# Performance work log

Hardware: AMD Instinct MI355X
Metric: run time of the kernel (lower is better)

## Reference

```python
import jax, jax.numpy as jnp
import numpy as np
import math

DIM = 768
NUM_HEADS = 12
HEAD_DIM = DIM // NUM_HEADS


def setup_inputs() -> dict:
    key = jax.random.key(0)
    k_x, k_q, k_k, k_v = jax.random.split(key, 4)
    s = 1.0 / math.sqrt(DIM)
    return {
        "x": jax.random.normal(k_x, (2, 2048, DIM), dtype=jnp.float32),
        "Wq": jax.random.normal(k_q, (DIM, DIM), dtype=jnp.float32) * s,
        "Wk": jax.random.normal(k_k, (DIM, DIM), dtype=jnp.float32) * s,
        "Wv": jax.random.normal(k_v, (DIM, DIM), dtype=jnp.float32) * s,
    }


def reference(x, Wq, Wk, Wv):
    b, n, _ = x.shape
    # nn.Linear(dim, dim, bias=False): y = x @ W.T
    def split_heads(y):
        return y.reshape(b, n, NUM_HEADS, HEAD_DIM).transpose(0, 2, 1, 3)  # b h n d
    Q = split_heads(x @ Wq.T)
    K = split_heads(x @ Wk.T)
    V = split_heads(x @ Wv.T)
    scores = jnp.einsum('bhqd,bhkd->bhqk', Q, K)
    # FAITHFUL to source: softmax over the HEADS axis (dim=1), then scale by 1/sqrt(dim)
    attn = jax.nn.softmax(scores, axis=1) / math.sqrt(DIM)
    out = jnp.einsum('bhqk,bhkd->bhqd', attn, V)
    out = out.transpose(0, 2, 1, 3).reshape(b, n, DIM)  # b n (h d)
    return out  # to_out is Identity (project_out=False)
```

## Files before the change

kernel.cpp:

```cpp
#include <hip/hip_runtime.h>

#define DIM 768
#define NHEADS 12
#define HDIM 64
#define BATCH 2
#define SEQ 2048
#define ROWS (BATCH*SEQ)
#define KSPLIT 4

typedef __attribute__((ext_vector_type(8))) _Float16 f16x8;
typedef __attribute__((ext_vector_type(4))) _Float16 f16x4;
typedef __attribute__((ext_vector_type(2))) _Float16 f16x2;
typedef __attribute__((ext_vector_type(4))) float    f32x4;

__device__ __forceinline__ void dma16(const _Float16* g, _Float16* l) {
    __builtin_amdgcn_global_load_lds(
        (const __attribute__((address_space(1))) unsigned int*)g,
        (__attribute__((address_space(3))) unsigned int*)l, 16, 0, 0);
}

__device__ __forceinline__ void barrier_lgkm() {
    asm volatile("s_waitcnt lgkmcnt(0)\n\ts_barrier" ::: "memory");
}


__global__ __launch_bounds__(256) void cvt_all(
    const float* __restrict__ x,  const float* __restrict__ wq,
    const float* __restrict__ wk, const float* __restrict__ wv,
    _Float16* __restrict__ xf,  _Float16* __restrict__ wqf,
    _Float16* __restrict__ wkf, _Float16* __restrict__ wvf)
{
    const int lane = threadIdx.x & 63;
    const int wid  = (blockIdx.x * 256 + threadIdx.x) >> 6;
    const float* src; _Float16* dst; int t;
    float sc = 1.0f;
    if (wid < 6144)      { src = x;  dst = xf;  t = wid;        }
    else if (wid < 7296) { src = wq; dst = wqf; t = wid - 6144; sc = 1.4426950408889634f; }
    else if (wid < 8448) { src = wk; dst = wkf; t = wid - 7296; }
    else                 { src = wv; dst = wvf; t = wid - 8448; }
    const int c = lane & 15, quad = lane >> 4;
    const int mt = t / 24, kt = t % 24;
    const float* p = src + (size_t)(mt*16 + c) * 768 + kt*32 + quad*8;
    float4 v0 = *(const float4*)p;
    float4 v1 = *(const float4*)(p + 4);
    f16x8 o;
    o[0]=(_Float16)(v0.x*sc); o[1]=(_Float16)(v0.y*sc); o[2]=(_Float16)(v0.z*sc); o[3]=(_Float16)(v0.w*sc);
    o[4]=(_Float16)(v1.x*sc); o[5]=(_Float16)(v1.y*sc); o[6]=(_Float16)(v1.z*sc); o[7]=(_Float16)(v1.w*sc);
    *reinterpret_cast<f16x8*>(dst + ((size_t)t * 64 + lane) * 8) = o;
}

__global__ __launch_bounds__(512) void gemm3(
    const _Float16* __restrict__ xf, const _Float16* __restrict__ wqkf,
    const _Float16* __restrict__ wvf,
    _Float16* __restrict__ Qf, _Float16* __restrict__ Kf, _Float16* __restrict__ Vkt)
{
    __shared__ _Float16 Ab[2][16*512];
    __shared__ _Float16 Bb[2][8*512];
    const int tid = threadIdx.x, lane = tid & 63, w = tid >> 6;
    const int c = lane & 15, quad = lane >> 4;

    const _Float16 *Af, *Bf;
    int mt0, nt0, mode;
    if ((int)blockIdx.x < 192) {
        int mt = blockIdx.x / 12, nt = blockIdx.x % 12;
        Af = xf; Bf = wqkf; mt0 = mt*16; nt0 = nt*8; mode = 0;
    } else {
        int v = blockIdx.x - 192;
        int mt = v / 32, nt = v % 32;
        Af = wvf; Bf = xf; mt0 = mt*16; nt0 = nt*8; mode = 1;
    }

    auto stage = [&](int kt, int buf) {
#pragma unroll
        for (int u = 0; u < 3; ++u) {
            const int cc = w*3 + u;
            const _Float16* s = (cc < 16) ? Af + ((size_t)(mt0+cc)*24 + kt)*512
                                          : Bf + ((size_t)(nt0+cc-16)*24 + kt)*512;
            _Float16* d = (cc < 16) ? &Ab[buf][cc*512] : &Bb[buf][(cc-16)*512];
            dma16(s + lane*8, d);
        }
    };

    stage(0, 0);
    __syncthreads();

    f32x4 acc[4][4] = {};
    for (int kt = 0; kt < 24; ++kt) {
        const int cur = kt & 1;
        if (kt < 23) stage(kt+1, cur^1);
        f16x8 a[4], b[4];
#pragma unroll
        for (int i = 0; i < 4; ++i)
            a[i] = *(const f16x8*)(&Ab[cur][((w>>1)*4 + i)*512] + lane*8);
#pragma unroll
        for (int j = 0; j < 4; ++j)
            b[j] = *(const f16x8*)(&Bb[cur][((w&1)*4 + j)*512] + lane*8);
#pragma unroll
        for (int i = 0; i < 4; ++i)
#pragma unroll
            for (int j = 0; j < 4; ++j)
                acc[i][j] = __builtin_amdgcn_mfma_f32_16x16x32_f16(a[i], b[j], acc[i][j], 0,0,0);
        __syncthreads();
    }

    _Float16* L = &Ab[0][0] + w*1280;
#pragma unroll
    for (int i2 = 0; i2 < 2; ++i2)
#pragma unroll
        for (int j2 = 0; j2 < 2; ++j2) {
#pragma unroll
            for (int ii = 0; ii < 2; ++ii)
#pragma unroll
                for (int jj = 0; jj < 2; ++jj)
#pragma unroll
                    for (int r = 0; r < 4; ++r)
                        L[(ii*16 + quad*4 + r)*40 + jj*16 + c] =
                            (_Float16)acc[i2*2+ii][j2*2+jj][r];
#pragma unroll
            for (int ii = 0; ii < 2; ++ii) {
                const int mtg = mt0 + (w>>1)*4 + i2*2 + ii;
                if (mode == 0) {
                    f16x8 v = *(const f16x8*)(L + (ii*16 + c)*40 + quad*8);
                    const int nt32 = (nt0 + (w&1)*4)/2 + j2;
                    _Float16* dst = (nt32 < 24)
                        ? Qf + ((size_t)(mtg*24 + nt32)*64 + lane)*8
                        : Kf + ((size_t)(mtg*24 + nt32 - 24)*64 + lane)*8;
                    *(f16x8*)dst = v;
                } else {
#pragma unroll
                    for (int jj = 0; jj < 2; ++jj) {
                        f16x4 v4 = *(const f16x4*)(L + (ii*16 + c)*40 + jj*16 + quad*4);
                        const int kcu = nt0 + (w&1)*4 + j2*2 + jj;
                        *(f16x4*)(Vkt + ((size_t)kcu*48 + mtg)*256 + lane*4) = v4;
                    }
                }
            }
        }
}

__global__ __launch_bounds__(512) __attribute__((amdgpu_waves_per_eu(4)))
void attn_kernel(
    const _Float16* __restrict__ Qf, const _Float16* __restrict__ Kf,
    const _Float16* __restrict__ Vkt,
    float* __restrict__ out,
    _Float16* __restrict__ part)
{
    __shared__ __attribute__((aligned(16))) float    Ps[8][336];
    __shared__ __attribute__((aligned(16))) _Float16 Pl[2][12][16][20];
    const int tid = threadIdx.x, lane = tid & 63, w = tid >> 6;
    const int c = lane & 15, quad = lane >> 4;
    const int qi = w >> 2, g = w & 3;

    const int bid = blockIdx.x;
    const int rb = (bid & 7)*64 + (bid >> 3);
    const int qb = rb & 63;
    const int ks = (rb >> 6) & 3;
    const int b  = rb >> 8;
    const int qrow0 = b*SEQ + qb*32;
    const int qt16  = (qrow0 >> 4) + qi;
    const int kb16  = (b*SEQ + ks*(SEQ/KSPLIT)) >> 4;
    const int psoff = quad*84 + c*4;

    f16x8 qreg[6];
#pragma unroll
    for (int u = 0; u < 6; ++u)
        qreg[u] = *(const f16x8*)(Qf + ((size_t)(qt16*24 + g*6 + u)*64 + lane)*8);

    const _Float16* Kp0 = Kf + ((size_t)kb16*24 + g*6)*512 + (size_t)lane*8;
    const _Float16* Vb0 = Vkt + ((size_t)kb16*48 + g)*256 + (size_t)lane*4;

    f32x4 o_acc[12] = {};
    f16x4 vv[12];
    f32x4 e3[3];

    for (int t = 0; t < 32; ++t) {
        const _Float16* Kpt = Kp0 + (size_t)t*24*512;
        f16x8 k0 = *(const f16x8*)(Kpt        );
        f16x8 k1 = *(const f16x8*)(Kpt +   512);
        f16x8 k2 = *(const f16x8*)(Kpt + 2*512);
        f16x8 k3 = *(const f16x8*)(Kpt + 3*512);
        f16x8 k4 = *(const f16x8*)(Kpt + 4*512);
        f16x8 k5 = *(const f16x8*)(Kpt + 5*512);
        {
            f32x4 a0 = {}, a1 = {}, a2 = {};
            a0 = __builtin_amdgcn_mfma_f32_16x16x32_f16(k0, qreg[0], a0, 0,0,0);
            a0 = __builtin_amdgcn_mfma_f32_16x16x32_f16(k1, qreg[1], a0, 0,0,0);
            a1 = __builtin_amdgcn_mfma_f32_16x16x32_f16(k2, qreg[2], a1, 0,0,0);
            a1 = __builtin_amdgcn_mfma_f32_16x16x32_f16(k3, qreg[3], a1, 0,0,0);
            a2 = __builtin_amdgcn_mfma_f32_16x16x32_f16(k4, qreg[4], a2, 0,0,0);
            a2 = __builtin_amdgcn_mfma_f32_16x16x32_f16(k5, qreg[5], a2, 0,0,0);
#pragma unroll
            for (int r = 0; r < 4; ++r) e3[0][r] = __builtin_amdgcn_exp2f(a0[r]);
#pragma unroll
            for (int r = 0; r < 4; ++r) e3[1][r] = __builtin_amdgcn_exp2f(a1[r]);
#pragma unroll
            for (int r = 0; r < 4; ++r) e3[2][r] = __builtin_amdgcn_exp2f(a2[r]);
        }
        {
            f32x4 ps;
#pragma unroll
            for (int r = 0; r < 4; ++r) ps[r] = e3[0][r] + e3[1][r] + e3[2][r];
            *(f32x4*)&Ps[qi*4+g][psoff] = ps;
        }
        if (t > 0) {
#pragma unroll
            for (int h = 0; h < 12; ++h) {
                f16x4 pf = *(const f16x4*)&Pl[qi][h][c][quad*4];
                o_acc[h] = __builtin_amdgcn_mfma_f32_16x16x16f16(vv[h], pf, o_acc[h], 0,0,0);
            }
        }
        barrier_lgkm();
#pragma unroll
        for (int h = 0; h < 12; ++h)
            vv[h] = *(const f16x4*)(Vb0 + ((size_t)t*48 + h*4)*256);
        {
            f32x4 s0 = *(const f32x4*)&Ps[qi*4+0][psoff];
            f32x4 s1 = *(const f32x4*)&Ps[qi*4+1][psoff];
            f32x4 s2 = *(const f32x4*)&Ps[qi*4+2][psoff];
            f32x4 s3 = *(const f32x4*)&Ps[qi*4+3][psoff];
            f32x4 inv;
#pragma unroll
            for (int r = 0; r < 4; ++r)
                inv[r] = __builtin_amdgcn_rcpf(
                    (s0[r]+s1[r]+s2[r]+s3[r]) * 27.712812921102035f);
#pragma unroll
            for (int hh = 0; hh < 3; ++hh) {
                f16x4 pw;
#pragma unroll
                for (int r = 0; r < 4; ++r) pw[r] = (_Float16)(e3[hh][r]*inv[r]);
                *(f16x4*)&Pl[qi][g*3+hh][c][quad*4] = pw;
            }
        }
        barrier_lgkm();
    }
#pragma unroll
    for (int h = 0; h < 12; ++h) {
        f16x4 pf = *(const f16x4*)&Pl[qi][h][c][quad*4];
        o_acc[h] = __builtin_amdgcn_mfma_f32_16x16x16f16(vv[h], pf, o_acc[h], 0,0,0);
    }

    if (ks == 0) {
#pragma unroll
        for (int h = 0; h < 12; ++h)
            *(f32x4*)(out + (size_t)(qrow0 + qi*16 + c)*DIM + h*64 + g*16 + quad*4)
                = o_acc[h];
    } else {
        _Float16* dst = part + (size_t)(ks - 1) * ROWS * DIM;
#pragma unroll
        for (int h = 0; h < 12; ++h) {
            f16x4 v;
#pragma unroll
            for (int r = 0; r < 4; ++r) v[r] = (_Float16)o_acc[h][r];
            *(f16x4*)(dst + (size_t)(qrow0 + qi*16 + c)*DIM + h*64 + g*16 + quad*4) = v;
        }
    }
}

__global__ __launch_bounds__(256) void reduce_add4(
    float* __restrict__ out, const _Float16* __restrict__ part, int n4)
{
    int i = blockIdx.x * 256 + threadIdx.x;
    if (i >= n4) return;
    float4 o = reinterpret_cast<float4*>(out)[i];
    const size_t N = (size_t)ROWS * DIM;
#pragma unroll
    for (int p = 0; p < 3; ++p) {
        f16x4 v = reinterpret_cast<const f16x4*>(part + p * N)[i];
        o.x += (float)v[0]; o.y += (float)v[1]; o.z += (float)v[2]; o.w += (float)v[3];
    }
    reinterpret_cast<float4*>(out)[i] = o;
}

extern "C" void kernel_launch(void* const* d_in, const int* in_sizes, int n_in,
                              void* d_out, int out_size, void* d_ws, size_t ws_size,
                              hipStream_t stream)
{
    const float* x  = (const float*)d_in[0];
    const float* Wq = (const float*)d_in[1];
    const float* Wk = (const float*)d_in[2];
    const float* Wv = (const float*)d_in[3];

    _Float16* ws  = (_Float16*)d_ws;
    const size_t XS = (size_t)ROWS * DIM;
    const size_t WS = (size_t)DIM * DIM;
    _Float16* xf   = ws;
    _Float16* wqf  = xf  + XS;
    _Float16* wkf  = wqf + WS;
    _Float16* wvf  = wkf + WS;
    _Float16* Qf   = wvf + WS;
    _Float16* Kf   = Qf  + XS;
    _Float16* Vkt  = Kf  + XS;
    _Float16* part = Vkt + XS;

    cvt_all<<<2400, 256, 0, stream>>>(x, Wq, Wk, Wv, xf, wqf, wkf, wvf);
    gemm3<<<288, 512, 0, stream>>>(xf, wqf, wvf, Qf, Kf, Vkt);
    attn_kernel<<<BATCH * KSPLIT * 64, 512, 0, stream>>>(
        Qf, Kf, Vkt, (float*)d_out, part);
    reduce_add4<<<(int)(XS/4 + 255)/256, 256, 0, stream>>>(
        (float*)d_out, part, (int)(XS/4));
}
```

Baseline: 214.1 us.

## Stage K tiles in LDS with double-buffered async global-to-LDS loads

Previously each wave read its K fragments straight from global memory, so the two query-tile waves sharing a K tile each fetched it. Now the block cooperatively DMAs each 24x512 K tile into a double-buffered LDS array with global_load_lds, prefetching the next tile while the current one is used. The QK MFMA and softmax partial-sum step moves after the V loads, and the end-of-iteration barrier becomes a full __syncthreads to protect buffer reuse. The cost is about 48 KB of extra LDS per block, which may lower occupancy, plus heavier synchronization.

```diff
diff --git a/kernel.cpp b/kernel.cpp
--- a/kernel.cpp
+++ b/kernel.cpp
@@ -145,6 +145,7 @@
     float* __restrict__ out,
     _Float16* __restrict__ part)
 {
+    __shared__ __attribute__((aligned(16))) _Float16 Kb[2][24*512];
     __shared__ __attribute__((aligned(16))) float    Ps[8][336];
     __shared__ __attribute__((aligned(16))) _Float16 Pl[2][12][16][20];
     const int tid = threadIdx.x, lane = tid & 63, w = tid >> 6;
@@ -166,41 +167,24 @@
     for (int u = 0; u < 6; ++u)
         qreg[u] = *(const f16x8*)(Qf + ((size_t)(qt16*24 + g*6 + u)*64 + lane)*8);
 
-    const _Float16* Kp0 = Kf + ((size_t)kb16*24 + g*6)*512 + (size_t)lane*8;
     const _Float16* Vb0 = Vkt + ((size_t)kb16*48 + g)*256 + (size_t)lane*4;
+
+#pragma unroll
+    for (int u = 0; u < 3; ++u)
+        dma16(Kf + ((size_t)kb16*24 + w*3 + u)*512 + lane*8, &Kb[0][(w*3+u)*512]);
+    __syncthreads();
 
     f32x4 o_acc[12] = {};
     f16x4 vv[12];
     f32x4 e3[3];
+    int cur = 0;
 
     for (int t = 0; t < 32; ++t) {
-        const _Float16* Kpt = Kp0 + (size_t)t*24*512;
-        f16x8 k0 = *(const f16x8*)(Kpt        );
-        f16x8 k1 = *(const f16x8*)(Kpt +   512);
-        f16x8 k2 = *(const f16x8*)(Kpt + 2*512);
-        f16x8 k3 = *(const f16x8*)(Kpt + 3*512);
-        f16x8 k4 = *(const f16x8*)(Kpt + 4*512);
-        f16x8 k5 = *(const f16x8*)(Kpt + 5*512);
-        {
-            f32x4 a0 = {}, a1 = {}, a2 = {};
-            a0 = __builtin_amdgcn_mfma_f32_16x16x32_f16(k0, qreg[0], a0, 0,0,0);
-            a0 = __builtin_amdgcn_mfma_f32_16x16x32_f16(k1, qreg[1], a0, 0,0,0);
-            a1 = __builtin_amdgcn_mfma_f32_16x16x32_f16(k2, qreg[2], a1, 0,0,0);
-            a1 = __builtin_amdgcn_mfma_f32_16x16x32_f16(k3, qreg[3], a1, 0,0,0);
-            a2 = __builtin_amdgcn_mfma_f32_16x16x32_f16(k4, qreg[4], a2, 0,0,0);
-            a2 = __builtin_amdgcn_mfma_f32_16x16x32_f16(k5, qreg[5], a2, 0,0,0);
-#pragma unroll
-            for (int r = 0; r < 4; ++r) e3[0][r] = __builtin_amdgcn_exp2f(a0[r]);
-#pragma unroll
-            for (int r = 0; r < 4; ++r) e3[1][r] = __builtin_amdgcn_exp2f(a1[r]);
-#pragma unroll
-            for (int r = 0; r < 4; ++r) e3[2][r] = __builtin_amdgcn_exp2f(a2[r]);
-        }
-        {
-            f32x4 ps;
-#pragma unroll
-            for (int r = 0; r < 4; ++r) ps[r] = e3[0][r] + e3[1][r] + e3[2][r];
-            *(f32x4*)&Ps[qi*4+g][psoff] = ps;
+        if (t < 31) {
+#pragma unroll
+            for (int u = 0; u < 3; ++u)
+                dma16(Kf + ((size_t)(kb16+t+1)*24 + w*3 + u)*512 + lane*8,
+                      &Kb[cur^1][(w*3+u)*512]);
         }
         if (t > 0) {
 #pragma unroll
@@ -209,10 +193,26 @@
                 o_acc[h] = __builtin_amdgcn_mfma_f32_16x16x16f16(vv[h], pf, o_acc[h], 0,0,0);
             }
         }
-        barrier_lgkm();
 #pragma unroll
         for (int h = 0; h < 12; ++h)
             vv[h] = *(const f16x4*)(Vb0 + ((size_t)t*48 + h*4)*256);
+#pragma unroll
+        for (int hh = 0; hh < 3; ++hh) {
+            f16x8 ka = *(const f16x8*)(&Kb[cur][(g*6 + hh*2    )*512] + lane*8);
+            f16x8 k2 = *(const f16x8*)(&Kb[cur][(g*6 + hh*2 + 1)*512] + lane*8);
+            f32x4 a = {};
+            a = __builtin_amdgcn_mfma_f32_16x16x32_f16(ka, qreg[hh*2],   a, 0,0,0);
+            a = __builtin_amdgcn_mfma_f32_16x16x32_f16(k2, qreg[hh*2+1], a, 0,0,0);
+#pragma unroll
+            for (int r = 0; r < 4; ++r) e3[hh][r] = __builtin_amdgcn_exp2f(a[r]);
+        }
+        {
+            f32x4 ps;
+#pragma unroll
+            for (int r = 0; r < 4; ++r) ps[r] = e3[0][r] + e3[1][r] + e3[2][r];
+            *(f32x4*)&Ps[qi*4+g][psoff] = ps;
+        }
+        barrier_lgkm();
         {
             f32x4 s0 = *(const f32x4*)&Ps[qi*4+0][psoff];
             f32x4 s1 = *(const f32x4*)&Ps[qi*4+1][psoff];
@@ -231,7 +231,8 @@
                 *(f16x4*)&Pl[qi][g*3+hh][c][quad*4] = pw;
             }
         }
-        barrier_lgkm();
+        __syncthreads();
+        cur ^= 1;
     }
 #pragma unroll
     for (int h = 0; h < 12; ++h) {
```

Result: faster. 200.5 us (-6.4%).
